# Performance work log

Measured on AMD Instinct MI355X. Metric: run time of the kernel, lower is better.

The kernel has to match this reference:

```python
import jax, jax.numpy as jnp
import numpy as np

B, S, IN_DIM, D, H, L = 2, 2048, 64, 512, 8, 2
DK = D // H
EPS = 1e-5

def _layernorm(x, g, b):
    mu = jnp.mean(x, axis=-1, keepdims=True)
    var = jnp.mean((x - mu) ** 2, axis=-1, keepdims=True)
    return (x - mu) * jax.lax.rsqrt(var + EPS) * g + b

def _prob_sparse_layer(x, Wq, bq, Wk, bk, Wv, bv, fcW, fcb, ln_g, ln_b):
    # x: [B, S, D]
    Bs, Ss, _ = x.shape
    Q = (x @ Wq + bq).reshape(Bs, Ss, H, DK).transpose(0, 2, 1, 3)  # [B,H,S,DK]
    K = (x @ Wk + bk).reshape(Bs, Ss, H, DK).transpose(0, 2, 1, 3)
    V = (x @ Wv + bv).reshape(Bs, Ss, H, DK).transpose(0, 2, 1, 3)
    scores = jnp.einsum('bhqd,bhkd->bhqk', Q, K) / np.sqrt(DK).astype(np.float32)
    k = max(1, Ss // 10)
    top_scores, _ = jax.lax.top_k(scores, k)          # [B,H,S,k]
    threshold = top_scores[..., -1:]                  # k-th largest per row
    sparse_scores = jnp.where(scores < threshold, -jnp.inf, scores)
    attn = jax.nn.softmax(sparse_scores, axis=-1)     # dropout is identity in eval
    out = jnp.einsum('bhqk,bhkd->bhqd', attn, V)
    out = out.transpose(0, 2, 1, 3).reshape(Bs, Ss, D)
    out = out @ fcW + fcb
    return _layernorm(x + out, ln_g, ln_b)

def setup_inputs() -> dict:
    key = jax.random.key(0)
    ks = jax.random.split(key, 16)
    sd = 1.0 / np.sqrt(D)
    sdi = 1.0 / np.sqrt(IN_DIM)
    return {
        'x': jax.random.normal(ks[0], (B, S, IN_DIM), jnp.float32),
        'enc_W': jax.random.normal(ks[1], (IN_DIM, D), jnp.float32) * sdi,
        'enc_b': jnp.zeros((D,), jnp.float32),
        'Wq': jax.random.normal(ks[2], (L, D, D), jnp.float32) * sd,
        'bq': jnp.zeros((L, D), jnp.float32),
        'Wk': jax.random.normal(ks[3], (L, D, D), jnp.float32) * sd,
        'bk': jnp.zeros((L, D), jnp.float32),
        'Wv': jax.random.normal(ks[4], (L, D, D), jnp.float32) * sd,
        'bv': jnp.zeros((L, D), jnp.float32),
        'fcW': jax.random.normal(ks[5], (L, D, D), jnp.float32) * sd,
        'fcb': jnp.zeros((L, D), jnp.float32),
        'ln_g': jnp.ones((L, D), jnp.float32),
        'ln_b': jnp.zeros((L, D), jnp.float32),
        'dec_W': jax.random.normal(ks[6], (D, IN_DIM), jnp.float32) * sd,
        'dec_b': jnp.zeros((IN_DIM,), jnp.float32),
    }

def reference(x, enc_W, enc_b, Wq, bq, Wk, bk, Wv, bv, fcW, fcb, ln_g, ln_b, dec_W, dec_b):
    h = x @ enc_W + enc_b  # [B,S,D]
    for i in range(Wq.shape[0]):
        h = _prob_sparse_layer(h, Wq[i], bq[i], Wk[i], bk[i], Wv[i], bv[i],
                               fcW[i], fcb[i], ln_g[i], ln_b[i])
    return h[:, -1, :] @ dec_W + dec_b  # [B, IN_DIM]
```

## Files before the change

### kernel.cpp

```cpp
#include <hip/hip_runtime.h>
#include <hip/hip_bf16.h>

typedef unsigned short u16;
typedef __bf16 bf16x8 __attribute__((ext_vector_type(8)));
typedef u16 u16x8 __attribute__((ext_vector_type(8)));
typedef float f32x4 __attribute__((ext_vector_type(4)));

#define S_LEN 2048
#define NH 8
#define DMODEL 512
#define TOPK 204

__device__ __forceinline__ u16 f2b(float f) {
  __hip_bfloat16 h = __float2bfloat16(f);
  return __builtin_bit_cast(u16, h);
}
__device__ __forceinline__ unsigned kmap16(u16 b) {
  return (unsigned)(u16)(b ^ ((b & 0x8000) ? 0xFFFFu : 0x8000u));
}
__device__ __forceinline__ float kunmap(unsigned k) {
  unsigned tb = (k & 0x8000u) ? (k ^ 0x8000u) : (~k & 0xFFFFu);
  return __uint_as_float(tb << 16);
}

__global__ void transpose_w(const float* __restrict__ in, u16* __restrict__ out, int R, int C) {
  __shared__ float tile[32][33];
  int c0 = blockIdx.x * 32, r0 = blockIdx.y * 32;
  int tx = threadIdx.x & 31, ty = threadIdx.x >> 5;
#pragma unroll
  for (int i = 0; i < 32; i += 8)
    tile[ty + i][tx] = in[(long long)(r0 + ty + i) * C + c0 + tx];
  __syncthreads();
#pragma unroll
  for (int i = 0; i < 32; i += 8)
    out[(long long)(c0 + ty + i) * R + r0 + tx] = f2b(tile[tx][ty + i]);
}

__global__ void transpose_w4(const float* __restrict__ W0, const float* __restrict__ W1,
                             const float* __restrict__ W2, const float* __restrict__ W3,
                             u16* __restrict__ O0, u16* __restrict__ O1,
                             u16* __restrict__ O2, u16* __restrict__ O3) {
  __shared__ float tile[32][33];
  const float* in;
  u16* out;
  switch (blockIdx.z) {
    case 0: in = W0; out = O0; break;
    case 1: in = W1; out = O1; break;
    case 2: in = W2; out = O2; break;
    default: in = W3; out = O3; break;
  }
  int c0 = blockIdx.x * 32, r0 = blockIdx.y * 32;
  int tx = threadIdx.x & 31, ty = threadIdx.x >> 5;
#pragma unroll
  for (int i = 0; i < 32; i += 8)
    tile[ty + i][tx] = in[(long long)(r0 + ty + i) * 512 + c0 + tx];
  __syncthreads();
#pragma unroll
  for (int i = 0; i < 32; i += 8)
    out[(long long)(c0 + ty + i) * 512 + r0 + tx] = f2b(tile[tx][ty + i]);
}

__global__ void conv_b(const float* __restrict__ in, u16* __restrict__ out, int n) {
  int i = blockIdx.x * 256 + threadIdx.x;
  if (i < n) out[i] = f2b(in[i]);
}

template <int MODE>
__global__ __launch_bounds__(256) void gemm_bt(
    const u16* __restrict__ A, const u16* __restrict__ BT,
    const float* __restrict__ bias, const float* __restrict__ biasK, const float* __restrict__ biasV,
    float* __restrict__ outF, u16* __restrict__ outB, u16* __restrict__ outBK, u16* __restrict__ outBV,
    int M, int N, int K, float scale) {
  __shared__ u16 As[64 * 32];
  __shared__ u16 Bs[128 * 32];
  int n0 = blockIdx.x * 128, m0 = blockIdx.y * 64;
  int t = threadIdx.x;
  int lane = t & 63, wv = t >> 6;
  int mw = (wv & 1) * 32, nw = (wv >> 1) * 64;
  int fr = lane & 15, fg = lane >> 4;
  f32x4 acc[2][4] = {};
  for (int kt = 0; kt < K; kt += 32) {
    int e0 = t * 8;
    int r0r = e0 >> 5, c0c = e0 & 31;
    int e1 = e0 + 2048;
    int r1r = e1 >> 5, c1c = e1 & 31;
    *(u16x8*)&As[e0] = *(const u16x8*)&A[(long long)(m0 + r0r) * K + kt + c0c];
    *(u16x8*)&Bs[e0] = *(const u16x8*)&BT[(long long)(n0 + r0r) * K + kt + c0c];
    *(u16x8*)&Bs[e1] = *(const u16x8*)&BT[(long long)(n0 + r1r) * K + kt + c1c];
    __syncthreads();
    bf16x8 af[2], bfv[4];
#pragma unroll
    for (int i = 0; i < 2; i++) af[i] = *(const bf16x8*)&As[(mw + i * 16 + fr) * 32 + fg * 8];
#pragma unroll
    for (int j = 0; j < 4; j++) bfv[j] = *(const bf16x8*)&Bs[(nw + j * 16 + fr) * 32 + fg * 8];
#pragma unroll
    for (int i = 0; i < 2; i++)
#pragma unroll
      for (int j = 0; j < 4; j++)
        acc[i][j] = __builtin_amdgcn_mfma_f32_16x16x32_bf16(af[i], bfv[j], acc[i][j], 0, 0, 0);
    __syncthreads();
  }
#pragma unroll
  for (int i = 0; i < 2; i++)
#pragma unroll
    for (int j = 0; j < 4; j++) {
      int mloc = mw + i * 16 + fg * 4;
      int n = n0 + nw + j * 16 + fr;
      float bvl;
      if constexpr (MODE == 5) {
        int seg = n >> 9, nn = n & 511;
        bvl = (seg == 0 ? bias : seg == 1 ? biasK : biasV)[nn];
      } else {
        bvl = bias ? bias[n] : 0.f;
      }
#pragma unroll
      for (int r = 0; r < 4; r++) {
        int m = m0 + mloc + r;
        float v = acc[i][j][r] * scale + bvl;
        if constexpr (MODE == 0) {
          outF[(long long)m * N + n] = v;
        } else if constexpr (MODE == 4) {
          outF[(long long)m * N + n] = v;
          outB[(long long)m * N + n] = f2b(v);
        } else if constexpr (MODE == 5) {
          int seg = n >> 9, nn = n & 511;
          u16 val = f2b(v);
          if (seg == 2) {
            outBV[((long long)((m >> 11) * NH + (nn >> 6)) * 64 + (nn & 63)) * S_LEN + (m & 2047)] = val;
          } else {
            long long qkidx = (long long)((m >> 11) * NH + (nn >> 6)) * (S_LEN * 64) +
                              (long long)(m & 2047) * 64 + (nn & 63);
            if (seg == 0) outB[qkidx] = val;
            else outBK[qkidx] = val;
          }
        }
      }
    }
}

__global__ __launch_bounds__(1024, 8) void score_pv(
    const u16* __restrict__ Qb, const u16* __restrict__ Kb, const u16* __restrict__ VTb,
    u16* __restrict__ aoB) {
  __shared__ u16 Qs[16 * 64];
  __shared__ __align__(16) u16 Ss[16 * 2048];
  __shared__ unsigned lokeyS[16];
  __shared__ float mS[16];
  __shared__ float zS[16 * 16];
  int bh = blockIdx.y, m0 = blockIdx.x * 16, t = threadIdx.x;
  int lane = t & 63, wv = t >> 6, fr = lane & 15, fg = lane >> 4;
  const u16* Qg = Qb + ((long long)bh * S_LEN + m0) * 64;
  const u16* Kg = Kb + (long long)bh * S_LEN * 64;
  const u16* Vg = VTb + (long long)bh * 64 * S_LEN;
  if (t < 128) {
    int row = t >> 3, cc = t & 7;
    *(u16x8*)&Qs[row * 64 + ((cc ^ (row & 7)) * 8)] = *(const u16x8*)&Qg[row * 64 + cc * 8];
  }
  __syncthreads();
  bf16x8 aq[2];
#pragma unroll
  for (int ks = 0; ks < 2; ks++)
    aq[ks] = *(const bf16x8*)&Qs[fr * 64 + (((fg + 4 * ks) ^ (fr & 7)) * 8)];

#pragma unroll 4
  for (int tt = 0; tt < 8; tt++) {
    int col0 = wv * 128 + tt * 16;
    f32x4 acc = {};
#pragma unroll
    for (int ks = 0; ks < 2; ks++) {
      bf16x8 bk = *(const bf16x8*)&Kg[(long long)(col0 + fr) * 64 + ks * 32 + fg * 8];
      acc = __builtin_amdgcn_mfma_f32_16x16x32_bf16(aq[ks], bk, acc, 0, 0, 0);
    }
#pragma unroll
    for (int r = 0; r < 4; r++) {
      float s = acc[r] * 0.125f;
      u16 key = (u16)kmap16(f2b(s));
      int row = fg * 4 + r;
      Ss[row * 2048 + ((col0 + fr) ^ ((row & 15) << 3))] = key;
    }
  }
  __syncthreads();

  {
    int rr = wv;
    const unsigned* cu = (const unsigned*)&Ss[rr * 2048];
    unsigned k32[32];
#pragma unroll
    for (int j = 0; j < 16; j++) {
      unsigned w = cu[lane + 64 * j];
      k32[2 * j] = w & 0xFFFFu;
      k32[2 * j + 1] = w >> 16;
    }
    unsigned mx = 0;
#pragma unroll
    for (int j = 0; j < 32; j++) mx = max(mx, k32[j]);
#pragma unroll
    for (int o = 1; o < 64; o <<= 1) mx = max(mx, (unsigned)__shfl_xor((int)mx, o));
    unsigned lo = 0, hi = mx;
    while (lo < hi) {
      unsigned mid = (lo + hi + 1) >> 1;
      int c = 0;
#pragma unroll
      for (int j = 0; j < 32; j++)
        c += (int)__popcll(__ballot(k32[j] >= mid));
      if (c >= TOPK) lo = mid; else hi = mid - 1;
    }
    if (lane == 0) {
      lokeyS[rr] = lo;
      mS[rr] = kunmap(mx);
    }
  }
  __syncthreads();

  unsigned myLo = lokeyS[fr];
  float myM = mS[fr];
  float zpart = 0.f;
  f32x4 acc_o[4] = {};
#pragma unroll 2
  for (int step = 0; step < 4; step++) {
    int k0 = wv * 128 + step * 32;
    u16x8 kk = *(const u16x8*)&Ss[fr * 2048 + ((k0 + fg * 8) ^ ((fr & 15) << 3))];
    u16x8 wpa;
#pragma unroll
    for (int e = 0; e < 8; e++) {
      unsigned key = kk[e];
      float pv = 0.f;
      if (key >= myLo) pv = __expf(kunmap(key) - myM);
      zpart += pv;
      wpa[e] = f2b(pv);
    }
    bf16x8 pa = *(bf16x8*)&wpa;
#pragma unroll
    for (int j = 0; j < 4; j++) {
      bf16x8 bv = *(const bf16x8*)&Vg[(long long)(j * 16 + fr) * 2048 + k0 + fg * 8];
      acc_o[j] = __builtin_amdgcn_mfma_f32_16x16x32_bf16(pa, bv, acc_o[j], 0, 0, 0);
    }
  }
  zpart += __shfl_xor(zpart, 16);
  zpart += __shfl_xor(zpart, 32);
  __syncthreads();

  float* Of = (float*)Ss;
#pragma unroll
  for (int j = 0; j < 4; j++)
#pragma unroll
    for (int r = 0; r < 4; r++) {
      int row = fg * 4 + r, col = j * 16 + fr;
      Of[wv * 1024 + row * 64 + (col ^ ((row >> 2) << 3))] = acc_o[j][r];
    }
  if (fg == 0) zS[wv * 16 + fr] = zpart;
  __syncthreads();
  long long ob = (long long)(bh >> 3) * S_LEN * DMODEL + (bh & 7) * 64;
  {
    int row = t >> 6, dk = t & 63;
    int sw = dk ^ ((row >> 2) << 3);
    float s = 0.f;
#pragma unroll
    for (int w = 0; w < 16; w++) s += Of[w * 1024 + row * 64 + sw];
    float z = 0.f;
#pragma unroll
    for (int w = 0; w < 16; w++) z += zS[w * 16 + row];
    aoB[ob + (long long)(m0 + row) * DMODEL + dk] = f2b(s / z);
  }
}

__global__ __launch_bounds__(256) void resid_ln(const float* __restrict__ h, const float* __restrict__ fco,
                                                const float* __restrict__ g, const float* __restrict__ b,
                                                float* __restrict__ hout, u16* __restrict__ hbout) {
  __shared__ float red[4];
  int row = blockIdx.x;
  int t = threadIdx.x;
  long long base = (long long)row * 512;
  float v0 = h[base + t] + fco[base + t];
  float v1 = h[base + t + 256] + fco[base + t + 256];
  float s = v0 + v1;
#pragma unroll
  for (int o = 32; o > 0; o >>= 1) s += __shfl_down(s, o);
  if ((t & 63) == 0) red[t >> 6] = s;
  __syncthreads();
  float mu = (red[0] + red[1] + red[2] + red[3]) * (1.f / 512.f);
  float d0 = v0 - mu, d1 = v1 - mu;
  float q = d0 * d0 + d1 * d1;
#pragma unroll
  for (int o = 32; o > 0; o >>= 1) q += __shfl_down(q, o);
  __syncthreads();
  if ((t & 63) == 0) red[t >> 6] = q;
  __syncthreads();
  float var = (red[0] + red[1] + red[2] + red[3]) * (1.f / 512.f);
  float rs = rsqrtf(var + 1e-5f);
  float y0 = d0 * rs * g[t] + b[t];
  float y1 = d1 * rs * g[t + 256] + b[t + 256];
  hout[base + t] = y0;
  hout[base + t + 256] = y1;
  hbout[base + t] = f2b(y0);
  hbout[base + t + 256] = f2b(y1);
}

__global__ void decoder_k(const float* __restrict__ h, const float* __restrict__ W,
                          const float* __restrict__ bias, float* __restrict__ out) {
  int t = threadIdx.x;
  int b = t >> 6, j = t & 63;
  const float* hr = h + ((long long)b * S_LEN + (S_LEN - 1)) * DMODEL;
  float s = 0.f;
  for (int d = 0; d < DMODEL; d++) s += hr[d] * W[(long long)d * 64 + j];
  out[t] = s + bias[j];
}

extern "C" void kernel_launch(void* const* d_in, const int* in_sizes, int n_in,
                              void* d_out, int out_size, void* d_ws, size_t ws_size,
                              hipStream_t stream) {
  const float* x = (const float*)d_in[0];
  const float* enc_W = (const float*)d_in[1];
  const float* enc_b = (const float*)d_in[2];
  const float* Wq = (const float*)d_in[3];
  const float* bq = (const float*)d_in[4];
  const float* Wk = (const float*)d_in[5];
  const float* bk = (const float*)d_in[6];
  const float* Wv = (const float*)d_in[7];
  const float* bv = (const float*)d_in[8];
  const float* fcW = (const float*)d_in[9];
  const float* fcb = (const float*)d_in[10];
  const float* ln_g = (const float*)d_in[11];
  const float* ln_b = (const float*)d_in[12];
  const float* dec_W = (const float*)d_in[13];
  const float* dec_b = (const float*)d_in[14];

  char* p = (char*)d_ws;
  auto alloc = [&](size_t bytes) {
    char* r = p;
    p += (bytes + 255) & ~(size_t)255;
    return r;
  };
  const size_t BS = 2 * (size_t)S_LEN;
  u16* encWT = (u16*)alloc(512 * 64 * 2);
  u16* xbf = (u16*)alloc(BS * 64 * 2);
  float* hF = (float*)alloc(BS * 512 * 4);
  u16* hB = (u16*)alloc(BS * 512 * 2);
  u16* WqT = (u16*)alloc(512 * 512 * 2);
  u16* WkT = (u16*)alloc(512 * 512 * 2);
  u16* WvT = (u16*)alloc(512 * 512 * 2);
  u16* fcWT = (u16*)alloc(512 * 512 * 2);
  u16* Qb = (u16*)alloc((size_t)16 * 2048 * 64 * 2);
  u16* Kb = (u16*)alloc((size_t)16 * 2048 * 64 * 2);
  u16* VTb = (u16*)alloc((size_t)16 * 2048 * 64 * 2);
  u16* aoB = (u16*)alloc(BS * 512 * 2);
  float* fcO = (float*)Qb;

  transpose_w<<<dim3(16, 2), 256, 0, stream>>>(enc_W, encWT, 64, 512);
  conv_b<<<(int)(BS * 64 / 256), 256, 0, stream>>>(x, xbf, (int)(BS * 64));
  gemm_bt<4><<<dim3(4, 64), 256, 0, stream>>>(xbf, encWT, enc_b, nullptr, nullptr,
                                              hF, hB, nullptr, nullptr, 4096, 512, 64, 1.f);

  for (int l = 0; l < 2; l++) {
    transpose_w4<<<dim3(16, 16, 4), 256, 0, stream>>>(
        Wq + (size_t)l * 512 * 512, Wk + (size_t)l * 512 * 512,
        Wv + (size_t)l * 512 * 512, fcW + (size_t)l * 512 * 512,
        WqT, WkT, WvT, fcWT);
    gemm_bt<5><<<dim3(12, 64), 256, 0, stream>>>(hB, WqT, bq + l * 512, bk + l * 512, bv + l * 512,
                                                 nullptr, Qb, Kb, VTb, 4096, 1536, 512, 1.f);
    score_pv<<<dim3(128, 16), 1024, 0, stream>>>(Qb, Kb, VTb, aoB);
    gemm_bt<0><<<dim3(4, 64), 256, 0, stream>>>(aoB, fcWT, fcb + l * 512, nullptr, nullptr,
                                                fcO, nullptr, nullptr, nullptr, 4096, 512, 512, 1.f);
    resid_ln<<<4096, 256, 0, stream>>>(hF, fcO, ln_g + l * 512, ln_b + l * 512, hF, hB);
  }
  decoder_k<<<1, 128, 0, stream>>>(hF, dec_W, dec_b, (float*)d_out);
}
```

Measured before the change: 411.5 us.

## Store raw bf16 scores, fold Q scaling into projection, narrow top-k bisection range

Moves the 1/sqrt(dk) scaling into the QKV projection epilogue, swaps the MFMA operand order so each lane writes four contiguous scores as one packed 8-byte store, and stores raw bf16 scores instead of order-mapped keys. The top-k threshold search now compares floats and first tests a window just below the row max to shrink the bisection range. Softmax weights use a hand-rolled round-to-nearest bf16 conversion. The goal is fewer ALU ops and LDS stores in the score and select phases, at the cost of an extra float conversion per bisection comparison, and the handmade rounding does not handle NaN.

```diff
diff --git a/kernel.cpp b/kernel.cpp
--- a/kernel.cpp
+++ b/kernel.cpp
@@ -15,12 +15,17 @@
   __hip_bfloat16 h = __float2bfloat16(f);
   return __builtin_bit_cast(u16, h);
 }
-__device__ __forceinline__ unsigned kmap16(u16 b) {
-  return (unsigned)(u16)(b ^ ((b & 0x8000) ? 0xFFFFu : 0x8000u));
+__device__ __forceinline__ unsigned f2b_fast(float f) {
+  unsigned u = __float_as_uint(f);
+  return (u + 0x7FFFu + ((u >> 16) & 1u)) >> 16;
 }
 __device__ __forceinline__ float kunmap(unsigned k) {
   unsigned tb = (k & 0x8000u) ? (k ^ 0x8000u) : (~k & 0xFFFFu);
   return __uint_as_float(tb << 16);
+}
+__device__ __forceinline__ unsigned fkmap(float f) {
+  unsigned b = __float_as_uint(f) >> 16;
+  return b ^ ((b & 0x8000u) ? 0xFFFFu : 0x8000u);
 }
 
 __global__ void transpose_w(const float* __restrict__ in, u16* __restrict__ out, int R, int C) {
@@ -124,6 +129,7 @@
           outB[(long long)m * N + n] = f2b(v);
         } else if constexpr (MODE == 5) {
           int seg = n >> 9, nn = n & 511;
+          if (seg == 0) v *= 0.125f;
           u16 val = f2b(v);
           if (seg == 2) {
             outBV[((long long)((m >> 11) * NH + (nn >> 6)) * 64 + (nn & 63)) * S_LEN + (m & 2047)] = val;
@@ -143,7 +149,7 @@
     u16* __restrict__ aoB) {
   __shared__ u16 Qs[16 * 64];
   __shared__ __align__(16) u16 Ss[16 * 2048];
-  __shared__ unsigned lokeyS[16];
+  __shared__ float thrS[16];
   __shared__ float mS[16];
   __shared__ float zS[16 * 16];
   int bh = blockIdx.y, m0 = blockIdx.x * 16, t = threadIdx.x;
@@ -168,50 +174,61 @@
 #pragma unroll
     for (int ks = 0; ks < 2; ks++) {
       bf16x8 bk = *(const bf16x8*)&Kg[(long long)(col0 + fr) * 64 + ks * 32 + fg * 8];
-      acc = __builtin_amdgcn_mfma_f32_16x16x32_bf16(aq[ks], bk, acc, 0, 0, 0);
-    }
-#pragma unroll
-    for (int r = 0; r < 4; r++) {
-      float s = acc[r] * 0.125f;
-      u16 key = (u16)kmap16(f2b(s));
-      int row = fg * 4 + r;
-      Ss[row * 2048 + ((col0 + fr) ^ ((row & 15) << 3))] = key;
-    }
+      acc = __builtin_amdgcn_mfma_f32_16x16x32_bf16(bk, aq[ks], acc, 0, 0, 0);
+    }
+    uint2 w;
+    w.x = f2b_fast(acc[0]) | (f2b_fast(acc[1]) << 16);
+    w.y = f2b_fast(acc[2]) | (f2b_fast(acc[3]) << 16);
+    int row = fr, col = col0 + fg * 4;
+    *(uint2*)&Ss[row * 2048 + (col ^ ((row & 15) << 3))] = w;
   }
   __syncthreads();
 
   {
     int rr = wv;
-    const unsigned* cu = (const unsigned*)&Ss[rr * 2048];
-    unsigned k32[32];
-#pragma unroll
-    for (int j = 0; j < 16; j++) {
-      unsigned w = cu[lane + 64 * j];
-      k32[2 * j] = w & 0xFFFFu;
-      k32[2 * j + 1] = w >> 16;
-    }
-    unsigned mx = 0;
-#pragma unroll
-    for (int j = 0; j < 32; j++) mx = max(mx, k32[j]);
-#pragma unroll
-    for (int o = 1; o < 64; o <<= 1) mx = max(mx, (unsigned)__shfl_xor((int)mx, o));
-    unsigned lo = 0, hi = mx;
+    const uint2* cu2 = (const uint2*)&Ss[rr * 2048];
+    float kf[32];
+#pragma unroll
+    for (int j = 0; j < 8; j++) {
+      uint2 w = cu2[lane + 64 * j];
+      kf[4 * j + 0] = __uint_as_float(w.x << 16);
+      kf[4 * j + 1] = __uint_as_float(w.x & 0xFFFF0000u);
+      kf[4 * j + 2] = __uint_as_float(w.y << 16);
+      kf[4 * j + 3] = __uint_as_float(w.y & 0xFFFF0000u);
+    }
+    float mxf = kf[0];
+#pragma unroll
+    for (int j = 1; j < 32; j++) mxf = fmaxf(mxf, kf[j]);
+#pragma unroll
+    for (int o = 1; o < 64; o <<= 1)
+      mxf = fmaxf(mxf, __uint_as_float((unsigned)__shfl_xor((int)__float_as_uint(mxf), o)));
+    unsigned mxi = fkmap(mxf);
+    unsigned lo, hi;
+    unsigned lo0 = mxi > 384u ? mxi - 384u : 0u;
+    {
+      float pf = kunmap(lo0);
+      int c = 0;
+#pragma unroll
+      for (int j = 0; j < 32; j++) c += (int)__popcll(__ballot(kf[j] >= pf));
+      if (c >= TOPK) { lo = lo0; hi = mxi; }
+      else { lo = 0u; hi = lo0 - 1u; }
+    }
     while (lo < hi) {
-      unsigned mid = (lo + hi + 1) >> 1;
+      unsigned mid = (lo + hi + 1u) >> 1;
+      float midf = kunmap(mid);
       int c = 0;
 #pragma unroll
-      for (int j = 0; j < 32; j++)
-        c += (int)__popcll(__ballot(k32[j] >= mid));
-      if (c >= TOPK) lo = mid; else hi = mid - 1;
+      for (int j = 0; j < 32; j++) c += (int)__popcll(__ballot(kf[j] >= midf));
+      if (c >= TOPK) lo = mid; else hi = mid - 1u;
     }
     if (lane == 0) {
-      lokeyS[rr] = lo;
-      mS[rr] = kunmap(mx);
-    }
-  }
-  __syncthreads();
-
-  unsigned myLo = lokeyS[fr];
+      thrS[rr] = kunmap(lo);
+      mS[rr] = mxf;
+    }
+  }
+  __syncthreads();
+
+  float thrF = thrS[fr];
   float myM = mS[fr];
   float zpart = 0.f;
   f32x4 acc_o[4] = {};
@@ -219,16 +236,17 @@
   for (int step = 0; step < 4; step++) {
     int k0 = wv * 128 + step * 32;
     u16x8 kk = *(const u16x8*)&Ss[fr * 2048 + ((k0 + fg * 8) ^ ((fr & 15) << 3))];
-    u16x8 wpa;
-#pragma unroll
-    for (int e = 0; e < 8; e++) {
-      unsigned key = kk[e];
-      float pv = 0.f;
-      if (key >= myLo) pv = __expf(kunmap(key) - myM);
-      zpart += pv;
-      wpa[e] = f2b(pv);
-    }
-    bf16x8 pa = *(bf16x8*)&wpa;
+    unsigned wp[4];
+#pragma unroll
+    for (int e2 = 0; e2 < 4; e2++) {
+      float s0 = __uint_as_float((unsigned)kk[2 * e2] << 16);
+      float s1 = __uint_as_float((unsigned)kk[2 * e2 + 1] << 16);
+      float p0 = (s0 >= thrF) ? __expf(s0 - myM) : 0.f;
+      float p1 = (s1 >= thrF) ? __expf(s1 - myM) : 0.f;
+      zpart += p0 + p1;
+      wp[e2] = f2b_fast(p0) | (f2b_fast(p1) << 16);
+    }
+    bf16x8 pa = *(bf16x8*)&wp;
 #pragma unroll
     for (int j = 0; j < 4; j++) {
       bf16x8 bv = *(const bf16x8*)&Vg[(long long)(j * 16 + fr) * 2048 + k0 + fg * 8];
```

After: 387.2 us. 1.06x faster.
